# Kernel optimization log

Measured on AMD Instinct MI355X. Metric: run time of the kernel, lower is better.

Reference implementation:

```python
import jax, jax.numpy as jnp
import numpy as np

B, W, F = 32, 100, 128   # batch, window_size, n_features
KSIZE = 7                # conv kernel size
EMB = 8                  # embedding dim for feature-similarity matrix
ALPHA = 0.2              # leaky relu negative slope


def setup_inputs() -> dict:
    key = jax.random.key(0)
    ks = jax.random.split(key, 10)
    s = 0.05
    return {
        "x": jax.random.normal(ks[0], (B, W, F), jnp.float32),
        # ConvLayer: Conv1d(F, F, KSIZE) with 'same' padding
        "conv_w": jax.random.normal(ks[1], (F, F, KSIZE), jnp.float32) * s,
        "conv_b": jnp.zeros((F,), jnp.float32),
        # TemporalAttentionLayer (GATv2): lin(2F -> 2F), a (2F,1), bias (W,W)
        "temp_lin_w": jax.random.normal(ks[2], (2 * F, 2 * F), jnp.float32) * s,
        "temp_lin_b": jnp.zeros((2 * F,), jnp.float32),
        "temp_a": jax.random.normal(ks[3], (2 * F, 1), jnp.float32) * s,
        "temp_bias": jnp.zeros((W, W), jnp.float32),
        # FeatureAttentionLayer (GATv2): lin(2W -> 2W), a (2W,1), bias (F,F)
        "feat_lin_w": jax.random.normal(ks[4], (2 * W, 2 * W), jnp.float32) * s,
        "feat_lin_b": jnp.zeros((2 * W,), jnp.float32),
        "feat_a": jax.random.normal(ks[5], (2 * W, 1), jnp.float32) * s,
        "feat_bias": jnp.zeros((F, F), jnp.float32),
        # nn.Embedding(F, EMB) table (indexed by arange(F) -> just the table)
        "emb": jax.random.normal(ks[6], (F, EMB), jnp.float32),
        # forecasting model: Linear(W, 1) + tanh
        "fc_w": jax.random.normal(ks[7], (1, W), jnp.float32) * s,
        "fc_b": jnp.zeros((1,), jnp.float32),
    }


def _pos_encode(x):
    # pe = sin(pos*div) + cos(pos*div), div = exp(arange(F) * -ln(1e4)/F)
    pos = jnp.arange(W, dtype=jnp.float32)[:, None]
    div = jnp.exp(jnp.arange(F, dtype=jnp.float32) * (-np.log(10000.0) / F))
    pe = jnp.sin(pos * div) + jnp.cos(pos * div)  # (W, F)
    return x + pe[None]


def _conv(x, w, b):
    # x: (B, W, F) -> Conv1d over time with channels = features, 'same' length
    xc = x.transpose(0, 2, 1)  # (B, F, W)
    pad = (KSIZE - 1) // 2
    y = jax.lax.conv_general_dilated(
        xc, w, window_strides=(1,), padding=[(pad, pad)],
        dimension_numbers=("NCW", "OIW", "NCW"))
    y = jax.nn.relu(y + b[None, :, None])
    return y.transpose(0, 2, 1)  # (B, W, F)


def _gat_v2(v, lin_w, lin_b, a, bias):
    # v: (B, K, D). Equivalent to lin(concat(v_i, v_j)) via split weights +
    # broadcast add (avoids the O(K^2) concat materialization).
    D = v.shape[-1]
    left = v @ lin_w[:, :D].T    # (B, K, E) -- v_i part
    right = v @ lin_w[:, D:].T   # (B, K, E) -- v_j part
    s = left[:, :, None, :] + right[:, None, :, :] + lin_b  # (B, K, K, E)
    s = jnp.where(s >= 0, s, ALPHA * s)  # leaky relu
    e = jnp.einsum("bije,e->bij", s, a[:, 0]) + bias  # (B, K, K)
    att = jax.nn.softmax(e, axis=2)
    return jnp.tanh(jnp.einsum("bij,bjd->bid", att, v))


def reference(x, conv_w, conv_b, temp_lin_w, temp_lin_b, temp_a, temp_bias,
              feat_lin_w, feat_lin_b, feat_a, feat_bias, emb, fc_w, fc_b):
    x = _pos_encode(x)                 # (B, W, F)
    x = _conv(x, conv_w, conv_b)       # (B, W, F)
    # temporal attention: nodes = time steps
    x = _gat_v2(x, temp_lin_w, temp_lin_b, temp_a, temp_bias)  # (B, W, F)
    # feature attention: nodes = features
    xf = x.transpose(0, 2, 1)          # (B, F, W)
    xf = _gat_v2(xf, feat_lin_w, feat_lin_b, feat_a, feat_bias)
    x = xf.transpose(0, 2, 1)          # (B, W, F)
    # cosine-similarity mixing over features
    norms = jnp.linalg.norm(emb, axis=-1)
    cos = (emb @ emb.T) / (norms[:, None] * norms[None, :])  # (F, F)
    x = x @ cos.T                      # (B, W, F)
    xp = x.transpose(0, 2, 1)          # (B, F, W)
    pred = jnp.tanh(xp @ fc_w.T + fc_b)  # (B, F, 1)
    return pred.transpose(0, 2, 1)     # (B, 1, F)
```

## Files before the change

### kernel.cpp

```cpp
#include <hip/hip_runtime.h>
#include <math.h>

#define BB 32
#define WW 100
#define FF 128
#define KS 7
#define ET 256
#define EF 200



__global__ void k_prep(const float* __restrict__ cw, const float* __restrict__ tlw,
                       const float* __restrict__ flw, float* __restrict__ wt,
                       float* __restrict__ tlwT, float* __restrict__ flwT) {
    int id = blockIdx.x * 256 + threadIdx.x;
    if (id < KS * FF * FF) {
        int o = id & (FF - 1);
        int r = id >> 7;
        int k = r % KS;
        int i = r / KS;
        wt[id] = cw[(o * FF + i) * KS + k];
    }
    if (id < ET * ET) {
        int e = id & (ET - 1);
        int d = id >> 8;
        tlwT[id] = tlw[e * ET + d];
    }
    if (id < EF * EF) {
        int e = id % EF;
        int d = id / EF;
        flwT[id] = flw[e * EF + d];
    }
}

#define CTW 10
#define NROW 16
#define XPAD 20
__global__ __launch_bounds__(512) void k_conv(const float* __restrict__ x,
                                              const float* __restrict__ wt,
                                              const float* __restrict__ cb,
                                              float* __restrict__ x2) {
    int b = blockIdx.x & 31;
    int tile = blockIdx.x >> 5;
    int w0 = tile * CTW;
    int tid = threadIdx.x;
    int o = tid & (FF - 1);
    int h = tid >> 7;
    __shared__ float xs[FF][XPAD];
    __shared__ float part[4][CTW][FF];
    for (int idx = tid; idx < NROW * FF; idx += 512) {
        int r = idx >> 7, f = idx & (FF - 1);
        int t = w0 - 3 + r;
        float v = 0.f;
        if ((unsigned)t < WW) {
            float div = __expf((float)f * (-9.210340371976184f / (float)FF));
            float arg = (float)t * div;
            v = x[(b * WW + t) * FF + f] + __sinf(arg) + __cosf(arg);
        }
        xs[f][r] = v;
    }
    __syncthreads();
    float acc[CTW];
#pragma unroll
    for (int t = 0; t < CTW; ++t) acc[t] = 0.f;
    const float* wbase = wt + (h * 32) * KS * FF + o;
#pragma unroll 2
    for (int il = 0; il < 32; ++il) {
        int i = h * 32 + il;
        float4 X0 = *(const float4*)&xs[i][0];
        float4 X1 = *(const float4*)&xs[i][4];
        float4 X2 = *(const float4*)&xs[i][8];
        float4 X3 = *(const float4*)&xs[i][12];
        float xr[16] = {X0.x, X0.y, X0.z, X0.w, X1.x, X1.y, X1.z, X1.w,
                        X2.x, X2.y, X2.z, X2.w, X3.x, X3.y, X3.z, X3.w};
        const float* wp = wbase + il * KS * FF;
#pragma unroll
        for (int k = 0; k < KS; ++k) {
            float wv = wp[k * FF];
#pragma unroll
            for (int t = 0; t < CTW; ++t) acc[t] += xr[t + k] * wv;
        }
    }
#pragma unroll
    for (int t = 0; t < CTW; ++t) part[h][t][o] = acc[t];
    __syncthreads();
    for (int idx = tid; idx < CTW * FF; idx += 512) {
        int t = idx >> 7, oo = idx & (FF - 1);
        float s = part[0][t][oo] + part[1][t][oo] + part[2][t][oo] +
                  part[3][t][oo] + cb[oo];
        x2[(b * WW + w0 + t) * FF + oo] = fmaxf(s, 0.f);
    }
}

__global__ __launch_bounds__(512) void k_lr_t(const float* __restrict__ x2,
                                              const float* __restrict__ tlwT,
                                              const float* __restrict__ tlb,
                                              float* __restrict__ LT,
                                              float* __restrict__ Rt) {
    int b = blockIdx.x & 31;
    int tile = blockIdx.x >> 5;
    int i0 = tile * 8;
    int tid = threadIdx.x;
    int e = tid & 255;
    int rh = tid >> 8;
    __shared__ float xs[8][FF];
    for (int idx = tid; idx < 8 * FF; idx += 512) {
        int r = idx >> 7, d = idx & (FF - 1);
        int row = i0 + r; if (row >= WW) row = WW - 1;
        xs[r][d] = x2[(b * WW + row) * FF + d];
    }
    __syncthreads();
    float aL[4] = {0, 0, 0, 0}, aR[4] = {0, 0, 0, 0};
    const float* wl = tlwT + e;
#pragma unroll 2
    for (int dc = 0; dc < 32; ++dc) {
        float xv[4][4];
#pragma unroll
        for (int r = 0; r < 4; ++r)
            *(float4*)xv[r] = *(const float4*)&xs[rh * 4 + r][dc * 4];
#pragma unroll
        for (int q = 0; q < 4; ++q) {
            int d = dc * 4 + q;
            float wL = wl[d * ET];
            float wR = wl[(FF + d) * ET];
#pragma unroll
            for (int r = 0; r < 4; ++r) {
                aL[r] += xv[r][q] * wL;
                aR[r] += xv[r][q] * wR;
            }
        }
    }
    int ibase = i0 + rh * 4;
    if (ibase < WW) {
        float lb = tlb[e];
        float o0[4];
#pragma unroll
        for (int r = 0; r < 4; ++r) o0[r] = aL[r] + lb;
        *(float4*)&LT[(b * ET + e) * WW + ibase] = *(float4*)o0;
        *(float4*)&Rt[(b * ET + e) * WW + ibase] = *(float4*)aR;
    }
}

__global__ __launch_bounds__(512) void k_att_t(const float* __restrict__ LT,
                                               const float* __restrict__ Rt,
                                               const float* __restrict__ ta,
                                               const float* __restrict__ tbias,
                                               const float* __restrict__ x2,
                                               float* __restrict__ x3T) {
    int b = blockIdx.x & 31;
    int tile = blockIdx.x >> 5;
    int i0 = tile * 8;
    int tid = threadIdx.x;
    int j = tid & 127, g = tid >> 7;
    __shared__ float Rs[32][FF];
    __shared__ float Ls[32][8];
    __shared__ float tas[ET];
    __shared__ float attQ[8][FF];
    __shared__ float ob[8][FF];
    __shared__ float redA[8][2], redB[8][2];
    if (tid < ET) tas[tid] = ta[tid];
    float s0 = 0.f, s1 = 0.f;
    for (int ch = 0; ch < 8; ++ch) {
        int e0 = ch * 32;
#pragma unroll
        for (int it = 0; it < 8; ++it) {
            int idx = tid + it * 512;
            int er = idx >> 7, w = idx & 127;
            Rs[er][w] = (w < WW) ? Rt[(b * ET + e0 + er) * WW + w] : 0.f;
        }
        if (tid < 256) {
            int er = tid >> 3, qq = tid & 7;
            int row = i0 + qq; if (row >= WW) row = WW - 1;
            Ls[er][qq] = LT[(b * ET + e0 + er) * WW + row];
        }
        __syncthreads();
#pragma unroll 8
        for (int e = 0; e < 32; ++e) {
            float rj = Rs[e][j];
            float ae = tas[e0 + e];
            float2 lv = *(const float2*)&Ls[e][g * 2];
            float v;
            v = lv.x + rj; v = fmaxf(v, 0.2f * v); s0 += v * ae;
            v = lv.y + rj; v = fmaxf(v, 0.2f * v); s1 += v * ae;
        }
        __syncthreads();
    }
    float ej[2];
#pragma unroll
    for (int ii = 0; ii < 2; ++ii) {
        int i = i0 + g * 2 + ii;
        float sv = (ii == 0) ? s0 : s1;
        float bv = (j < WW && i < WW) ? tbias[i * WW + j] : 0.f;
        ej[ii] = (j < WW && i < WW) ? sv + bv : -1e30f;
    }
    float m[2] = {ej[0], ej[1]};
#pragma unroll
    for (int off = 32; off > 0; off >>= 1) {
#pragma unroll
        for (int ii = 0; ii < 2; ++ii) m[ii] = fmaxf(m[ii], __shfl_xor(m[ii], off));
    }
    int wv = tid >> 6;
    if ((tid & 63) == 0) { redA[wv][0] = m[0]; redA[wv][1] = m[1]; }
    __syncthreads();
    float p[2], ps[2];
#pragma unroll
    for (int ii = 0; ii < 2; ++ii) {
        float mx = fmaxf(redA[g * 2][ii], redA[g * 2 + 1][ii]);
        p[ii] = (j < WW) ? __expf(ej[ii] - mx) : 0.f;
        ps[ii] = p[ii];
    }
#pragma unroll
    for (int off = 32; off > 0; off >>= 1) {
#pragma unroll
        for (int ii = 0; ii < 2; ++ii) ps[ii] += __shfl_xor(ps[ii], off);
    }
    if ((tid & 63) == 0) { redB[wv][0] = ps[0]; redB[wv][1] = ps[1]; }
    __syncthreads();
#pragma unroll
    for (int ii = 0; ii < 2; ++ii) {
        float inv = 1.f / (redB[g * 2][ii] + redB[g * 2 + 1][ii]);
        attQ[g * 2 + ii][j] = p[ii] * inv;
    }
    int d = tid & 127, ph = tid >> 7;
    float pv0 = 0.f, pv1 = 0.f;
    const float* a0 = attQ[ph * 2];
    const float* a1 = attQ[ph * 2 + 1];
    for (int jc = 0; jc < 4; ++jc) {
        __syncthreads();
        for (int idx = tid; idx < 25 * FF; idx += 512) {
            int r = idx >> 7, f = idx & 127;
            Rs[r][f] = x2[(b * WW + jc * 25 + r) * FF + f];
        }
        __syncthreads();
#pragma unroll 5
        for (int r = 0; r < 25; ++r) {
            float xv = Rs[r][d];
            pv0 += a0[jc * 25 + r] * xv;
            pv1 += a1[jc * 25 + r] * xv;
        }
    }
    ob[ph * 2][d] = tanhf(pv0);
    ob[ph * 2 + 1][d] = tanhf(pv1);
    __syncthreads();
    if (tid < 256) {
        int f = tid >> 1, half = tid & 1;
        if (i0 + half * 4 < WW) {
            float4 v = make_float4(ob[half * 4][f], ob[half * 4 + 1][f],
                                   ob[half * 4 + 2][f], ob[half * 4 + 3][f]);
            *(float4*)&x3T[(b * FF + f) * WW + i0 + half * 4] = v;
        }
    }
}

__global__ __launch_bounds__(512) void k_lr_f(const float* __restrict__ x3T,
                                              const float* __restrict__ flwT,
                                              const float* __restrict__ flb,
                                              float* __restrict__ LfT,
                                              float* __restrict__ RfT) {
    int b = blockIdx.x & 31;
    int tile = blockIdx.x >> 5;
    int f0 = tile * 8;
    int tid = threadIdx.x;
    int e = tid & 255;
    int rh = tid >> 8;
    __shared__ float xs[8][WW];
    for (int idx = tid; idx < 8 * WW; idx += 512) {
        int r = idx / WW, d = idx % WW;
        xs[r][d] = x3T[(b * FF + f0 + r) * WW + d];
    }
    __syncthreads();
    if (e < EF) {
        float aL[4] = {0, 0, 0, 0}, aR[4] = {0, 0, 0, 0};
        const float* wl = flwT + e;
#pragma unroll 2
        for (int dc = 0; dc < 25; ++dc) {
            float xv[4][4];
#pragma unroll
            for (int r = 0; r < 4; ++r)
                *(float4*)xv[r] = *(const float4*)&xs[rh * 4 + r][dc * 4];
#pragma unroll
            for (int q = 0; q < 4; ++q) {
                int d = dc * 4 + q;
                float wL = wl[d * EF];
                float wR = wl[(WW + d) * EF];
#pragma unroll
                for (int r = 0; r < 4; ++r) {
                    aL[r] += xv[r][q] * wL;
                    aR[r] += xv[r][q] * wR;
                }
            }
        }
        float lb = flb[e];
        float o0[4];
#pragma unroll
        for (int r = 0; r < 4; ++r) o0[r] = aL[r] + lb;
        int fbase = f0 + rh * 4;
        *(float4*)&LfT[(b * EF + e) * FF + fbase] = *(float4*)o0;
        *(float4*)&RfT[(b * EF + e) * FF + fbase] = *(float4*)aR;
    }
}

__global__ __launch_bounds__(512) void k_att_f(const float* __restrict__ LfT,
                                               const float* __restrict__ RfT,
                                               const float* __restrict__ fa,
                                               const float* __restrict__ fbias,
                                               const float* __restrict__ x3T,
                                               const float* __restrict__ fcw,
                                               float* __restrict__ tj) {
    int b = blockIdx.x & 31;
    int tile = blockIdx.x >> 5;
    int f0 = tile * 8;
    int tid = threadIdx.x;
    int j = tid & 127, g = tid >> 7;
    __shared__ float Rs[32][FF];
    __shared__ float Ls[25][8];
    __shared__ float fas[EF];
    __shared__ float attQ[8][FF];
    __shared__ float redA[8][2], redB[8][2], redT[8][2];
    if (tid < EF) fas[tid] = fa[tid];
    float s0 = 0.f, s1 = 0.f;
    for (int ch = 0; ch < 8; ++ch) {
        int e0 = ch * 25;
        for (int idx = tid; idx < 25 * FF; idx += 512) {
            int er = idx >> 7, f = idx & 127;
            Rs[er][f] = RfT[(b * EF + e0 + er) * FF + f];
        }
        if (tid < 200) {
            int er = tid >> 3, qq = tid & 7;
            Ls[er][qq] = LfT[(b * EF + e0 + er) * FF + f0 + qq];
        }
        __syncthreads();
#pragma unroll 5
        for (int e = 0; e < 25; ++e) {
            float rj = Rs[e][j];
            float ae = fas[e0 + e];
            float2 lv = *(const float2*)&Ls[e][g * 2];
            float v;
            v = lv.x + rj; v = fmaxf(v, 0.2f * v); s0 += v * ae;
            v = lv.y + rj; v = fmaxf(v, 0.2f * v); s1 += v * ae;
        }
        __syncthreads();
    }
    float ej[2] = {s0 + fbias[(f0 + g * 2) * FF + j],
                   s1 + fbias[(f0 + g * 2 + 1) * FF + j]};
    float m[2] = {ej[0], ej[1]};
#pragma unroll
    for (int off = 32; off > 0; off >>= 1) {
#pragma unroll
        for (int ii = 0; ii < 2; ++ii) m[ii] = fmaxf(m[ii], __shfl_xor(m[ii], off));
    }
    int wv = tid >> 6;
    if ((tid & 63) == 0) { redA[wv][0] = m[0]; redA[wv][1] = m[1]; }
    __syncthreads();
    float p[2], ps[2];
#pragma unroll
    for (int ii = 0; ii < 2; ++ii) {
        float mx = fmaxf(redA[g * 2][ii], redA[g * 2 + 1][ii]);
        p[ii] = __expf(ej[ii] - mx);
        ps[ii] = p[ii];
    }
#pragma unroll
    for (int off = 32; off > 0; off >>= 1) {
#pragma unroll
        for (int ii = 0; ii < 2; ++ii) ps[ii] += __shfl_xor(ps[ii], off);
    }
    if ((tid & 63) == 0) { redB[wv][0] = ps[0]; redB[wv][1] = ps[1]; }
    __syncthreads();
#pragma unroll
    for (int ii = 0; ii < 2; ++ii) {
        float inv = 1.f / (redB[g * 2][ii] + redB[g * 2 + 1][ii]);
        attQ[g * 2 + ii][j] = p[ii] * inv;
    }
    int w = tid & 127, ph = tid >> 7;
    float pv0 = 0.f, pv1 = 0.f;
    const float* a0 = attQ[ph * 2];
    const float* a1 = attQ[ph * 2 + 1];
    for (int jc = 0; jc < 4; ++jc) {
        __syncthreads();
#pragma unroll
        for (int it = 0; it < 8; ++it) {
            int idx = tid + it * 512;
            int r = idx >> 7, ww = idx & 127;
            Rs[r][ww] = (ww < WW) ? x3T[(b * FF + jc * 32 + r) * WW + ww] : 0.f;
        }
        __syncthreads();
#pragma unroll 8
        for (int r = 0; r < 32; ++r) {
            float xv = Rs[r][w];
            pv0 += a0[jc * 32 + r] * xv;
            pv1 += a1[jc * 32 + r] * xv;
        }
    }
    bool wok = (w < WW);
    float fcv = wok ? fcw[w] : 0.f;
    float tv[2] = {tanhf(pv0) * fcv, tanhf(pv1) * fcv};
#pragma unroll
    for (int off = 32; off > 0; off >>= 1) {
#pragma unroll
        for (int ii = 0; ii < 2; ++ii) tv[ii] += __shfl_xor(tv[ii], off);
    }
    if ((tid & 63) == 0) { redT[wv][0] = tv[0]; redT[wv][1] = tv[1]; }
    __syncthreads();
    if (tid < 8) {
        int q = tid, php = q >> 1, ii = q & 1;
        tj[b * FF + f0 + q] = redT[php * 2][ii] + redT[php * 2 + 1][ii];
    }
}

__global__ __launch_bounds__(128) void k_fc(const float* __restrict__ tjg,
                                            const float* __restrict__ emb,
                                            const float* __restrict__ fcb,
                                            float* __restrict__ out) {
    int b = blockIdx.x;
    int f = threadIdx.x;
    __shared__ float en[FF][12];
    __shared__ float tjs[FF];
    {
        float4 e0 = *(const float4*)&emb[f * 8];
        float4 e1 = *(const float4*)&emb[f * 8 + 4];
        float n = e0.x*e0.x + e0.y*e0.y + e0.z*e0.z + e0.w*e0.w +
                  e1.x*e1.x + e1.y*e1.y + e1.z*e1.z + e1.w*e1.w;
        float rin = rsqrtf(n);
        float4 a = make_float4(e0.x*rin, e0.y*rin, e0.z*rin, e0.w*rin);
        float4 c = make_float4(e1.x*rin, e1.y*rin, e1.z*rin, e1.w*rin);
        *(float4*)&en[f][0] = a;
        *(float4*)&en[f][4] = c;
        tjs[f] = tjg[b * FF + f];
    }
    __syncthreads();
    float er[8];
#pragma unroll
    for (int k = 0; k < 8; ++k) er[k] = en[f][k];
    float acc = fcb[0];
    for (int jj = 0; jj < FF; ++jj) {
        float4 a = *(const float4*)&en[jj][0];
        float4 c = *(const float4*)&en[jj][4];
        float d8 = er[0]*a.x + er[1]*a.y + er[2]*a.z + er[3]*a.w +
                   er[4]*c.x + er[5]*c.y + er[6]*c.z + er[7]*c.w;
        acc += d8 * tjs[jj];
    }
    out[b * FF + f] = tanhf(acc);
}

extern "C" void kernel_launch(void* const* d_in, const int* in_sizes, int n_in,
                              void* d_out, int out_size, void* d_ws, size_t ws_size,
                              hipStream_t stream) {
    const float* x     = (const float*)d_in[0];
    const float* cw    = (const float*)d_in[1];
    const float* cb    = (const float*)d_in[2];
    const float* tlw   = (const float*)d_in[3];
    const float* tlb   = (const float*)d_in[4];
    const float* ta    = (const float*)d_in[5];
    const float* tbias = (const float*)d_in[6];
    const float* flw   = (const float*)d_in[7];
    const float* flb   = (const float*)d_in[8];
    const float* fa    = (const float*)d_in[9];
    const float* fbias = (const float*)d_in[10];
    const float* emb   = (const float*)d_in[11];
    const float* fcw   = (const float*)d_in[12];
    const float* fcb   = (const float*)d_in[13];
    float* out = (float*)d_out;
    float* ws = (float*)d_ws;

    float* x2   = ws + 409600;
    float* x3T  = ws + 819200;
    float* LT   = ws + 1228800;
    float* Rt   = ws + 2048000;
    float* tj   = ws + 2867200;
    float* wt   = ws + 3297280;
    float* tlwT = ws + 3411968;
    float* flwT = ws + 3477504;

    k_prep<<<448, 256, 0, stream>>>(cw, tlw, flw, wt, tlwT, flwT);
    k_conv<<<BB * 10, 512, 0, stream>>>(x, wt, cb, x2);
    k_lr_t<<<BB * 13, 512, 0, stream>>>(x2, tlwT, tlb, LT, Rt);
    k_att_t<<<BB * 13, 512, 0, stream>>>(LT, Rt, ta, tbias, x2, x3T);
    k_lr_f<<<BB * 16, 512, 0, stream>>>(x3T, flwT, flb, LT, Rt);
    k_att_f<<<BB * 16, 512, 0, stream>>>(LT, Rt, fa, fbias, x3T, fcw, tj);
    k_fc<<<BB, 128, 0, stream>>>(tj, emb, fcb, out);
}
```

Measured before the change: 127.6 us.

## Split attention score reduction across e-dimension with per-thread 8-row register tiles

In both attention kernels each thread now computes all 8 query rows for one column j over a quarter of the embedding dimension, instead of 2 rows over the full dimension. Partial sums are combined through a shared-memory buffer. The attention-times-values product gets the same treatment, reading a transposed attention matrix as float4 and reducing row partials across thread groups. This raises arithmetic per shared-memory load of Rs, at the cost of extra shared memory, extra barriers, and softmax work confined to 128 threads.

After: 138.9 us. +8.9%, slower.

```diff
diff --git a/kernel.cpp b/kernel.cpp
--- a/kernel.cpp
+++ b/kernel.cpp
@@ -7,7 +7,6 @@
 #define KS 7
 #define ET 256
 #define EF 200
-
 
 
 __global__ void k_prep(const float* __restrict__ cw, const float* __restrict__ tlw,
@@ -151,15 +150,16 @@
     int tile = blockIdx.x >> 5;
     int i0 = tile * 8;
     int tid = threadIdx.x;
-    int j = tid & 127, g = tid >> 7;
+    int j = tid & 127, eq = tid >> 7;
     __shared__ float Rs[32][FF];
     __shared__ float Ls[32][8];
     __shared__ float tas[ET];
-    __shared__ float attQ[8][FF];
+    __shared__ float sacc[4][8][128];
+    __shared__ float attQT[WW][8];
     __shared__ float ob[8][FF];
-    __shared__ float redA[8][2], redB[8][2];
+    __shared__ float redM[2][8], redS[2][8];
     if (tid < ET) tas[tid] = ta[tid];
-    float s0 = 0.f, s1 = 0.f;
+    float s[8] = {0, 0, 0, 0, 0, 0, 0, 0};
     for (int ch = 0; ch < 8; ++ch) {
         int e0 = ch * 32;
 #pragma unroll
@@ -174,57 +174,78 @@
             Ls[er][qq] = LT[(b * ET + e0 + er) * WW + row];
         }
         __syncthreads();
-#pragma unroll 8
-        for (int e = 0; e < 32; ++e) {
+#pragma unroll
+        for (int el = 0; el < 8; ++el) {
+            int e = eq * 8 + el;
             float rj = Rs[e][j];
             float ae = tas[e0 + e];
-            float2 lv = *(const float2*)&Ls[e][g * 2];
+            float4 l0 = *(const float4*)&Ls[e][0];
+            float4 l1 = *(const float4*)&Ls[e][4];
             float v;
-            v = lv.x + rj; v = fmaxf(v, 0.2f * v); s0 += v * ae;
-            v = lv.y + rj; v = fmaxf(v, 0.2f * v); s1 += v * ae;
-        }
-        __syncthreads();
-    }
-    float ej[2];
-#pragma unroll
-    for (int ii = 0; ii < 2; ++ii) {
-        int i = i0 + g * 2 + ii;
-        float sv = (ii == 0) ? s0 : s1;
-        float bv = (j < WW && i < WW) ? tbias[i * WW + j] : 0.f;
-        ej[ii] = (j < WW && i < WW) ? sv + bv : -1e30f;
-    }
-    float m[2] = {ej[0], ej[1]};
+            v = l0.x + rj; v = fmaxf(v, 0.2f * v); s[0] += v * ae;
+            v = l0.y + rj; v = fmaxf(v, 0.2f * v); s[1] += v * ae;
+            v = l0.z + rj; v = fmaxf(v, 0.2f * v); s[2] += v * ae;
+            v = l0.w + rj; v = fmaxf(v, 0.2f * v); s[3] += v * ae;
+            v = l1.x + rj; v = fmaxf(v, 0.2f * v); s[4] += v * ae;
+            v = l1.y + rj; v = fmaxf(v, 0.2f * v); s[5] += v * ae;
+            v = l1.z + rj; v = fmaxf(v, 0.2f * v); s[6] += v * ae;
+            v = l1.w + rj; v = fmaxf(v, 0.2f * v); s[7] += v * ae;
+        }
+        __syncthreads();
+    }
+#pragma unroll
+    for (int q = 0; q < 8; ++q) sacc[eq][q][j] = s[q];
+    __syncthreads();
+    bool act = tid < 128;
+    float ej[8];
+#pragma unroll
+    for (int q = 0; q < 8; ++q) {
+        float v = -1e30f;
+        if (act) {
+            int i = i0 + q;
+            v = sacc[0][q][j] + sacc[1][q][j] + sacc[2][q][j] + sacc[3][q][j];
+            v += (j < WW && i < WW) ? tbias[i * WW + j] : 0.f;
+            if (j >= WW) v = -1e30f;
+        }
+        ej[q] = v;
+    }
+    float m[8];
+#pragma unroll
+    for (int q = 0; q < 8; ++q) m[q] = ej[q];
 #pragma unroll
     for (int off = 32; off > 0; off >>= 1) {
 #pragma unroll
-        for (int ii = 0; ii < 2; ++ii) m[ii] = fmaxf(m[ii], __shfl_xor(m[ii], off));
-    }
-    int wv = tid >> 6;
-    if ((tid & 63) == 0) { redA[wv][0] = m[0]; redA[wv][1] = m[1]; }
-    __syncthreads();
-    float p[2], ps[2];
-#pragma unroll
-    for (int ii = 0; ii < 2; ++ii) {
-        float mx = fmaxf(redA[g * 2][ii], redA[g * 2 + 1][ii]);
-        p[ii] = (j < WW) ? __expf(ej[ii] - mx) : 0.f;
-        ps[ii] = p[ii];
+        for (int q = 0; q < 8; ++q) m[q] = fmaxf(m[q], __shfl_xor(m[q], off));
+    }
+    if (act && (tid & 63) == 0) {
+#pragma unroll
+        for (int q = 0; q < 8; ++q) redM[tid >> 6][q] = m[q];
+    }
+    __syncthreads();
+    float p[8], ps[8];
+#pragma unroll
+    for (int q = 0; q < 8; ++q) {
+        float mx = fmaxf(redM[0][q], redM[1][q]);
+        p[q] = (act && j < WW) ? __expf(ej[q] - mx) : 0.f;
+        ps[q] = p[q];
     }
 #pragma unroll
     for (int off = 32; off > 0; off >>= 1) {
 #pragma unroll
-        for (int ii = 0; ii < 2; ++ii) ps[ii] += __shfl_xor(ps[ii], off);
-    }
-    if ((tid & 63) == 0) { redB[wv][0] = ps[0]; redB[wv][1] = ps[1]; }
-    __syncthreads();
-#pragma unroll
-    for (int ii = 0; ii < 2; ++ii) {
-        float inv = 1.f / (redB[g * 2][ii] + redB[g * 2 + 1][ii]);
-        attQ[g * 2 + ii][j] = p[ii] * inv;
-    }
-    int d = tid & 127, ph = tid >> 7;
-    float pv0 = 0.f, pv1 = 0.f;
-    const float* a0 = attQ[ph * 2];
-    const float* a1 = attQ[ph * 2 + 1];
+        for (int q = 0; q < 8; ++q) ps[q] += __shfl_xor(ps[q], off);
+    }
+    if (act && (tid & 63) == 0) {
+#pragma unroll
+        for (int q = 0; q < 8; ++q) redS[tid >> 6][q] = ps[q];
+    }
+    __syncthreads();
+    if (act && j < WW) {
+#pragma unroll
+        for (int q = 0; q < 8; ++q)
+            attQT[j][q] = p[q] / (redS[0][q] + redS[1][q]);
+    }
+    int d = j, rq = eq;
+    float pv[8] = {0, 0, 0, 0, 0, 0, 0, 0};
     for (int jc = 0; jc < 4; ++jc) {
         __syncthreads();
         for (int idx = tid; idx < 25 * FF; idx += 512) {
@@ -232,15 +253,27 @@
             Rs[r][f] = x2[(b * WW + jc * 25 + r) * FF + f];
         }
         __syncthreads();
-#pragma unroll 5
-        for (int r = 0; r < 25; ++r) {
+        for (int r = rq; r < 25; r += 4) {
             float xv = Rs[r][d];
-            pv0 += a0[jc * 25 + r] * xv;
-            pv1 += a1[jc * 25 + r] * xv;
-        }
-    }
-    ob[ph * 2][d] = tanhf(pv0);
-    ob[ph * 2 + 1][d] = tanhf(pv1);
+            float4 a0 = *(const float4*)&attQT[jc * 25 + r][0];
+            float4 a1 = *(const float4*)&attQT[jc * 25 + r][4];
+            pv[0] += a0.x * xv; pv[1] += a0.y * xv;
+            pv[2] += a0.z * xv; pv[3] += a0.w * xv;
+            pv[4] += a1.x * xv; pv[5] += a1.y * xv;
+            pv[6] += a1.z * xv; pv[7] += a1.w * xv;
+        }
+    }
+    __syncthreads();
+#pragma unroll
+    for (int q = 0; q < 8; ++q) sacc[rq][q][d] = pv[q];
+    __syncthreads();
+    if (tid < 128) {
+#pragma unroll
+        for (int q = 0; q < 8; ++q) {
+            float v = sacc[0][q][d] + sacc[1][q][d] + sacc[2][q][d] + sacc[3][q][d];
+            ob[q][d] = tanhf(v);
+        }
+    }
     __syncthreads();
     if (tid < 256) {
         int f = tid >> 1, half = tid & 1;
@@ -311,70 +344,96 @@
     int tile = blockIdx.x >> 5;
     int f0 = tile * 8;
     int tid = threadIdx.x;
-    int j = tid & 127, g = tid >> 7;
-    __shared__ float Rs[32][FF];
-    __shared__ float Ls[25][8];
+    int j = tid & 127, eq = tid >> 7;
+    __shared__ float Rs[40][FF];
+    __shared__ float Ls[40][8];
     __shared__ float fas[EF];
-    __shared__ float attQ[8][FF];
-    __shared__ float redA[8][2], redB[8][2], redT[8][2];
+    __shared__ float sacc[4][8][128];
+    __shared__ float attQT[FF][8];
+    __shared__ float redM[2][8], redS[2][8], redT[2][8];
     if (tid < EF) fas[tid] = fa[tid];
-    float s0 = 0.f, s1 = 0.f;
-    for (int ch = 0; ch < 8; ++ch) {
-        int e0 = ch * 25;
-        for (int idx = tid; idx < 25 * FF; idx += 512) {
+    float s[8] = {0, 0, 0, 0, 0, 0, 0, 0};
+    for (int ch = 0; ch < 5; ++ch) {
+        int e0 = ch * 40;
+        for (int idx = tid; idx < 40 * FF; idx += 512) {
             int er = idx >> 7, f = idx & 127;
             Rs[er][f] = RfT[(b * EF + e0 + er) * FF + f];
         }
-        if (tid < 200) {
+        if (tid < 320) {
             int er = tid >> 3, qq = tid & 7;
             Ls[er][qq] = LfT[(b * EF + e0 + er) * FF + f0 + qq];
         }
         __syncthreads();
-#pragma unroll 5
-        for (int e = 0; e < 25; ++e) {
+#pragma unroll
+        for (int el = 0; el < 10; ++el) {
+            int e = eq * 10 + el;
             float rj = Rs[e][j];
             float ae = fas[e0 + e];
-            float2 lv = *(const float2*)&Ls[e][g * 2];
+            float4 l0 = *(const float4*)&Ls[e][0];
+            float4 l1 = *(const float4*)&Ls[e][4];
             float v;
-            v = lv.x + rj; v = fmaxf(v, 0.2f * v); s0 += v * ae;
-            v = lv.y + rj; v = fmaxf(v, 0.2f * v); s1 += v * ae;
-        }
-        __syncthreads();
-    }
-    float ej[2] = {s0 + fbias[(f0 + g * 2) * FF + j],
-                   s1 + fbias[(f0 + g * 2 + 1) * FF + j]};
-    float m[2] = {ej[0], ej[1]};
+            v = l0.x + rj; v = fmaxf(v, 0.2f * v); s[0] += v * ae;
+            v = l0.y + rj; v = fmaxf(v, 0.2f * v); s[1] += v * ae;
+            v = l0.z + rj; v = fmaxf(v, 0.2f * v); s[2] += v * ae;
+            v = l0.w + rj; v = fmaxf(v, 0.2f * v); s[3] += v * ae;
+            v = l1.x + rj; v = fmaxf(v, 0.2f * v); s[4] += v * ae;
+            v = l1.y + rj; v = fmaxf(v, 0.2f * v); s[5] += v * ae;
+            v = l1.z + rj; v = fmaxf(v, 0.2f * v); s[6] += v * ae;
+            v = l1.w + rj; v = fmaxf(v, 0.2f * v); s[7] += v * ae;
+        }
+        __syncthreads();
+    }
+#pragma unroll
+    for (int q = 0; q < 8; ++q) sacc[eq][q][j] = s[q];
+    __syncthreads();
+    bool act = tid < 128;
+    float ej[8];
+#pragma unroll
+    for (int q = 0; q < 8; ++q) {
+        float v = -1e30f;
+        if (act) {
+            v = sacc[0][q][j] + sacc[1][q][j] + sacc[2][q][j] + sacc[3][q][j];
+            v += fbias[(f0 + q) * FF + j];
+        }
+        ej[q] = v;
+    }
+    float m[8];
+#pragma unroll
+    for (int q = 0; q < 8; ++q) m[q] = ej[q];
 #pragma unroll
     for (int off = 32; off > 0; off >>= 1) {
 #pragma unroll
-        for (int ii = 0; ii < 2; ++ii) m[ii] = fmaxf(m[ii], __shfl_xor(m[ii], off));
-    }
-    int wv = tid >> 6;
-    if ((tid & 63) == 0) { redA[wv][0] = m[0]; redA[wv][1] = m[1]; }
-    __syncthreads();
-    float p[2], ps[2];
-#pragma unroll
-    for (int ii = 0; ii < 2; ++ii) {
-        float mx = fmaxf(redA[g * 2][ii], redA[g * 2 + 1][ii]);
-        p[ii] = __expf(ej[ii] - mx);
-        ps[ii] = p[ii];
+        for (int q = 0; q < 8; ++q) m[q] = fmaxf(m[q], __shfl_xor(m[q], off));
+    }
+    if (act && (tid & 63) == 0) {
+#pragma unroll
+        for (int q = 0; q < 8; ++q) redM[tid >> 6][q] = m[q];
+    }
+    __syncthreads();
+    float p[8], ps[8];
+#pragma unroll
+    for (int q = 0; q < 8; ++q) {
+        float mx = fmaxf(redM[0][q], redM[1][q]);
+        p[q] = act ? __expf(ej[q] - mx) : 0.f;
+        ps[q] = p[q];
     }
 #pragma unroll
     for (int off = 32; off > 0; off >>= 1) {
 #pragma unroll
-        for (int ii = 0; ii < 2; ++ii) ps[ii] += __shfl_xor(ps[ii], off);
-    }
-    if ((tid & 63) == 0) { redB[wv][0] = ps[0]; redB[wv][1] = ps[1]; }
-    __syncthreads();
-#pragma unroll
-    for (int ii = 0; ii < 2; ++ii) {
-        float inv = 1.f / (redB[g * 2][ii] + redB[g * 2 + 1][ii]);
-        attQ[g * 2 + ii][j] = p[ii] * inv;
-    }
-    int w = tid & 127, ph = tid >> 7;
-    float pv0 = 0.f, pv1 = 0.f;
-    const float* a0 = attQ[ph * 2];
-    const float* a1 = attQ[ph * 2 + 1];
+        for (int q = 0; q < 8; ++q) ps[q] += __shfl_xor(ps[q], off);
+    }
+    if (act && (tid & 63) == 0) {
+#pragma unroll
+        for (int q = 0; q < 8; ++q) redS[tid >> 6][q] = ps[q];
+    }
+    __syncthreads();
+    if (act) {
+#pragma unroll
+        for (int q = 0; q < 8; ++q)
+            attQT[j][q] = p[q] / (redS[0][q] + redS[1][q]);
+    }
+    int w = j, rq = eq;
+    float pv[8] = {0, 0, 0, 0, 0, 0, 0, 0};
     for (int jc = 0; jc < 4; ++jc) {
         __syncthreads();
 #pragma unroll
@@ -384,27 +443,42 @@
             Rs[r][ww] = (ww < WW) ? x3T[(b * FF + jc * 32 + r) * WW + ww] : 0.f;
         }
         __syncthreads();
-#pragma unroll 8
-        for (int r = 0; r < 32; ++r) {
+#pragma unroll
+        for (int rr = 0; rr < 8; ++rr) {
+            int r = rq * 8 + rr;
             float xv = Rs[r][w];
-            pv0 += a0[jc * 32 + r] * xv;
-            pv1 += a1[jc * 32 + r] * xv;
-        }
-    }
-    bool wok = (w < WW);
+            float4 a0 = *(const float4*)&attQT[jc * 32 + r][0];
+            float4 a1 = *(const float4*)&attQT[jc * 32 + r][4];
+            pv[0] += a0.x * xv; pv[1] += a0.y * xv;
+            pv[2] += a0.z * xv; pv[3] += a0.w * xv;
+            pv[4] += a1.x * xv; pv[5] += a1.y * xv;
+            pv[6] += a1.z * xv; pv[7] += a1.w * xv;
+        }
+    }
+    __syncthreads();
+#pragma unroll
+    for (int q = 0; q < 8; ++q) sacc[rq][q][w] = pv[q];
+    __syncthreads();
+    float tv[8];
+    bool wok = act && (w < WW);
     float fcv = wok ? fcw[w] : 0.f;
-    float tv[2] = {tanhf(pv0) * fcv, tanhf(pv1) * fcv};
+#pragma unroll
+    for (int q = 0; q < 8; ++q) {
+        float v = act ? (sacc[0][q][w] + sacc[1][q][w] + sacc[2][q][w] + sacc[3][q][w]) : 0.f;
+        tv[q] = act ? tanhf(v) * fcv : 0.f;
+    }
 #pragma unroll
     for (int off = 32; off > 0; off >>= 1) {
 #pragma unroll
-        for (int ii = 0; ii < 2; ++ii) tv[ii] += __shfl_xor(tv[ii], off);
-    }
-    if ((tid & 63) == 0) { redT[wv][0] = tv[0]; redT[wv][1] = tv[1]; }
-    __syncthreads();
-    if (tid < 8) {
-        int q = tid, php = q >> 1, ii = q & 1;
-        tj[b * FF + f0 + q] = redT[php * 2][ii] + redT[php * 2 + 1][ii];
-    }
+        for (int q = 0; q < 8; ++q) tv[q] += __shfl_xor(tv[q], off);
+    }
+    if (act && (tid & 63) == 0) {
+#pragma unroll
+        for (int q = 0; q < 8; ++q) redT[tid >> 6][q] = tv[q];
+    }
+    __syncthreads();
+    if (tid < 8)
+        tj[b * FF + f0 + tid] = redT[0][tid] + redT[1][tid];
 }
 
 __global__ __launch_bounds__(128) void k_fc(const float* __restrict__ tjg,
```

## Double-buffer shared-memory tiles with register prefetch in attention kernels

Applied to the files above, without the earlier changes.

The temporal and feature attention kernels now stage the next chunk of R/L rows and x rows into registers while the current chunk is computed from a second shared-memory buffer. This halves the barriers per chunk and overlaps global loads with the score and aggregation loops. The feature kernel also moves to 40-row chunks, and the temporal aggregation moves to 32-row chunks. The cost is more shared memory and registers per 512-thread block, which may lower occupancy.

After: 118.2 us, median of 3. 1.08x faster.

```diff
diff --git a/kernel.cpp b/kernel.cpp
--- a/kernel.cpp
+++ b/kernel.cpp
@@ -7,7 +7,6 @@
 #define KS 7
 #define ET 256
 #define EF 200
-
 
 
 __global__ void k_prep(const float* __restrict__ cw, const float* __restrict__ tlw,
@@ -152,46 +151,84 @@
     int i0 = tile * 8;
     int tid = threadIdx.x;
     int j = tid & 127, g = tid >> 7;
-    __shared__ float Rs[32][FF];
-    __shared__ float Ls[32][8];
+    __shared__ float Rs[2][32][FF];
+    __shared__ float Ls[2][32][8];
     __shared__ float tas[ET];
     __shared__ float attQ[8][FF];
     __shared__ float ob[8][FF];
     __shared__ float redA[8][2], redB[8][2];
     if (tid < ET) tas[tid] = ta[tid];
-    float s0 = 0.f, s1 = 0.f;
-    for (int ch = 0; ch < 8; ++ch) {
-        int e0 = ch * 32;
+
+    float rv[8];
+    float lvr = 0.f;
+    {
+        const float* Rb = Rt + (b * ET) * WW;
 #pragma unroll
         for (int it = 0; it < 8; ++it) {
             int idx = tid + it * 512;
             int er = idx >> 7, w = idx & 127;
-            Rs[er][w] = (w < WW) ? Rt[(b * ET + e0 + er) * WW + w] : 0.f;
+            rv[it] = (w < WW) ? Rb[er * WW + w] : 0.f;
         }
         if (tid < 256) {
             int er = tid >> 3, qq = tid & 7;
             int row = i0 + qq; if (row >= WW) row = WW - 1;
-            Ls[er][qq] = LT[(b * ET + e0 + er) * WW + row];
-        }
-        __syncthreads();
+            lvr = LT[(b * ET + er) * WW + row];
+        }
+    }
+#pragma unroll
+    for (int it = 0; it < 8; ++it) {
+        int idx = tid + it * 512;
+        Rs[0][idx >> 7][idx & 127] = rv[it];
+    }
+    if (tid < 256) Ls[0][tid >> 3][tid & 7] = lvr;
+    __syncthreads();
+
+    float s0 = 0.f, s1 = 0.f;
+    for (int ch = 0; ch < 8; ++ch) {
+        int buf = ch & 1;
+        if (ch < 7) {
+            int e0 = (ch + 1) * 32;
+            const float* Rb = Rt + (b * ET + e0) * WW;
+#pragma unroll
+            for (int it = 0; it < 8; ++it) {
+                int idx = tid + it * 512;
+                int er = idx >> 7, w = idx & 127;
+                rv[it] = (w < WW) ? Rb[er * WW + w] : 0.f;
+            }
+            if (tid < 256) {
+                int er = tid >> 3, qq = tid & 7;
+                int row = i0 + qq; if (row >= WW) row = WW - 1;
+                lvr = LT[(b * ET + e0 + er) * WW + row];
+            }
+        }
+        int e0 = ch * 32;
 #pragma unroll 8
         for (int e = 0; e < 32; ++e) {
-            float rj = Rs[e][j];
+            float rj = Rs[buf][e][j];
             float ae = tas[e0 + e];
-            float2 lv = *(const float2*)&Ls[e][g * 2];
+            float2 lv2 = *(const float2*)&Ls[buf][e][g * 2];
             float v;
-            v = lv.x + rj; v = fmaxf(v, 0.2f * v); s0 += v * ae;
-            v = lv.y + rj; v = fmaxf(v, 0.2f * v); s1 += v * ae;
+            v = lv2.x + rj; v = fmaxf(v, 0.2f * v); s0 += v * ae;
+            v = lv2.y + rj; v = fmaxf(v, 0.2f * v); s1 += v * ae;
+        }
+        if (ch < 7) {
+#pragma unroll
+            for (int it = 0; it < 8; ++it) {
+                int idx = tid + it * 512;
+                Rs[buf ^ 1][idx >> 7][idx & 127] = rv[it];
+            }
+            if (tid < 256) Ls[buf ^ 1][tid >> 3][tid & 7] = lvr;
         }
         __syncthreads();
     }
+
     float ej[2];
-#pragma unroll
-    for (int ii = 0; ii < 2; ++ii) {
-        int i = i0 + g * 2 + ii;
-        float sv = (ii == 0) ? s0 : s1;
-        float bv = (j < WW && i < WW) ? tbias[i * WW + j] : 0.f;
-        ej[ii] = (j < WW && i < WW) ? sv + bv : -1e30f;
+    {
+        int iq = i0 + g * 2;
+        float bv0 = (j < WW && iq < WW) ? tbias[iq * WW + j] : 0.f;
+        float bv1 = (j < WW && iq + 1 < WW) ? tbias[(iq + 1) * WW + j] : 0.f;
+        ej[0] = (j < WW && iq < WW) ? s0 + bv0 : -1e30f;
+        ej[1] = (j < WW && iq + 1 < WW) ? s1 + bv1 : -1e30f;
     }
     float m[2] = {ej[0], ej[1]};
 #pragma unroll
@@ -221,23 +258,51 @@
         float inv = 1.f / (redB[g * 2][ii] + redB[g * 2 + 1][ii]);
         attQ[g * 2 + ii][j] = p[ii] * inv;
     }
-    int d = tid & 127, ph = tid >> 7;
+
+    int d = j, ph = g;
     float pv0 = 0.f, pv1 = 0.f;
+#pragma unroll
+    for (int it = 0; it < 8; ++it) {
+        int idx = tid + it * 512;
+        int r = idx >> 7, f = idx & 127;
+        rv[it] = (r < WW) ? x2[(b * WW + r) * FF + f] : 0.f;
+    }
+    __syncthreads();
+#pragma unroll
+    for (int it = 0; it < 8; ++it) {
+        int idx = tid + it * 512;
+        Rs[0][idx >> 7][idx & 127] = rv[it];
+    }
+    __syncthreads();
     const float* a0 = attQ[ph * 2];
     const float* a1 = attQ[ph * 2 + 1];
     for (int jc = 0; jc < 4; ++jc) {
+        int buf = jc & 1;
+        if (jc < 3) {
+            int r0 = (jc + 1) * 32;
+#pragma unroll
+            for (int it = 0; it < 8; ++it) {
+                int idx = tid + it * 512;
+                int r = idx >> 7, f = idx & 127;
+                int row = r0 + r;
+                rv[it] = (row < WW) ? x2[(b * WW + row) * FF + f] : 0.f;
+            }
+        }
+#pragma unroll 8
+        for (int r = 0; r < 32; ++r) {
+            float xv = Rs[buf][r][d];
+            int row = jc * 32 + r;
+            pv0 += a0[row] * xv;
+            pv1 += a1[row] * xv;
+        }
+        if (jc < 3) {
+#pragma unroll
+            for (int it = 0; it < 8; ++it) {
+                int idx = tid + it * 512;
+                Rs[buf ^ 1][idx >> 7][idx & 127] = rv[it];
+            }
+        }
         __syncthreads();
-        for (int idx = tid; idx < 25 * FF; idx += 512) {
-            int r = idx >> 7, f = idx & 127;
-            Rs[r][f] = x2[(b * WW + jc * 25 + r) * FF + f];
-        }
-        __syncthreads();
-#pragma unroll 5
-        for (int r = 0; r < 25; ++r) {
-            float xv = Rs[r][d];
-            pv0 += a0[jc * 25 + r] * xv;
-            pv1 += a1[jc * 25 + r] * xv;
-        }
     }
     ob[ph * 2][d] = tanhf(pv0);
     ob[ph * 2 + 1][d] = tanhf(pv1);
@@ -312,35 +377,72 @@
     int f0 = tile * 8;
     int tid = threadIdx.x;
     int j = tid & 127, g = tid >> 7;
-    __shared__ float Rs[32][FF];
-    __shared__ float Ls[25][8];
+    __shared__ float Rs[2][40][FF];
+    __shared__ float Ls[2][40][8];
     __shared__ float fas[EF];
     __shared__ float attQ[8][FF];
     __shared__ float redA[8][2], redB[8][2], redT[8][2];
     if (tid < EF) fas[tid] = fa[tid];
+
+    float rv[10];
+    float lvr = 0.f;
+    {
+        const float* Rb = RfT + (b * EF) * FF;
+#pragma unroll
+        for (int it = 0; it < 10; ++it) {
+            int idx = tid + it * 512;
+            rv[it] = Rb[idx];
+        }
+        if (tid < 320) {
+            int er = tid >> 3, qq = tid & 7;
+            lvr = LfT[(b * EF + er) * FF + f0 + qq];
+        }
+    }
+#pragma unroll
+    for (int it = 0; it < 10; ++it) {
+        int idx = tid + it * 512;
+        Rs[0][idx >> 7][idx & 127] = rv[it];
+    }
+    if (tid < 320) Ls[0][tid >> 3][tid & 7] = lvr;
+    __syncthreads();
+
     float s0 = 0.f, s1 = 0.f;
-    for (int ch = 0; ch < 8; ++ch) {
-        int e0 = ch * 25;
-        for (int idx = tid; idx < 25 * FF; idx += 512) {
-            int er = idx >> 7, f = idx & 127;
-            Rs[er][f] = RfT[(b * EF + e0 + er) * FF + f];
-        }
-        if (tid < 200) {
-            int er = tid >> 3, qq = tid & 7;
-            Ls[er][qq] = LfT[(b * EF + e0 + er) * FF + f0 + qq];
+    for (int ch = 0; ch < 5; ++ch) {
+        int buf = ch & 1;
+        if (ch < 4) {
+            int e0 = (ch + 1) * 40;
+            const float* Rb = RfT + (b * EF + e0) * FF;
+#pragma unroll
+            for (int it = 0; it < 10; ++it) {
+                int idx = tid + it * 512;
+                rv[it] = Rb[idx];
+            }
+            if (tid < 320) {
+                int er = tid >> 3, qq = tid & 7;
+                lvr = LfT[(b * EF + e0 + er) * FF + f0 + qq];
+            }
+        }
+        int e0 = ch * 40;
+#pragma unroll 8
+        for (int e = 0; e < 40; ++e) {
+            float rj = Rs[buf][e][j];
+            float ae = fas[e0 + e];
+            float2 lv2 = *(const float2*)&Ls[buf][e][g * 2];
+            float v;
+            v = lv2.x + rj; v = fmaxf(v, 0.2f * v); s0 += v * ae;
+            v = lv2.y + rj; v = fmaxf(v, 0.2f * v); s1 += v * ae;
+        }
+        if (ch < 4) {
+#pragma unroll
+            for (int it = 0; it < 10; ++it) {
+                int idx = tid + it * 512;
+                Rs[buf ^ 1][idx >> 7][idx & 127] = rv[it];
+            }
+            if (tid < 320) Ls[buf ^ 1][tid >> 3][tid & 7] = lvr;
         }
         __syncthreads();
-#pragma unroll 5
-        for (int e = 0; e < 25; ++e) {
-            float rj = Rs[e][j];
-            float ae = fas[e0 + e];
-            float2 lv = *(const float2*)&Ls[e][g * 2];
-            float v;
-            v = lv.x + rj; v = fmaxf(v, 0.2f * v); s0 += v * ae;
-            v = lv.y + rj; v = fmaxf(v, 0.2f * v); s1 += v * ae;
-        }
-        __syncthreads();
-    }
+    }
+
     float ej[2] = {s0 + fbias[(f0 + g * 2) * FF + j],
                    s1 + fbias[(f0 + g * 2 + 1) * FF + j]};
     float m[2] = {ej[0], ej[1]};
@@ -371,25 +473,50 @@
         float inv = 1.f / (redB[g * 2][ii] + redB[g * 2 + 1][ii]);
         attQ[g * 2 + ii][j] = p[ii] * inv;
     }
-    int w = tid & 127, ph = tid >> 7;
+
+    int w = j, ph = g;
     float pv0 = 0.f, pv1 = 0.f;
+#pragma unroll
+    for (int it = 0; it < 8; ++it) {
+        int idx = tid + it * 512;
+        int r = idx >> 7, ww = idx & 127;
+        rv[it] = (ww < WW) ? x3T[(b * FF + r) * WW + ww] : 0.f;
+    }
+    __syncthreads();
+#pragma unroll
+    for (int it = 0; it < 8; ++it) {
+        int idx = tid + it * 512;
+        Rs[0][idx >> 7][idx & 127] = rv[it];
+    }
+    __syncthreads();
     const float* a0 = attQ[ph * 2];
     const float* a1 = attQ[ph * 2 + 1];
     for (int jc = 0; jc < 4; ++jc) {
-        __syncthreads();
-#pragma unroll
-        for (int it = 0; it < 8; ++it) {
-            int idx = tid + it * 512;
-            int r = idx >> 7, ww = idx & 127;
-            Rs[r][ww] = (ww < WW) ? x3T[(b * FF + jc * 32 + r) * WW + ww] : 0.f;
-        }
-        __syncthreads();
+        int buf = jc & 1;
+        if (jc < 3) {
+            int r0 = (jc + 1) * 32;
+#pragma unroll
+            for (int it = 0; it < 8; ++it) {
+                int idx = tid + it * 512;
+                int r = idx >> 7, ww = idx & 127;
+                rv[it] = (ww < WW) ? x3T[(b * FF + r0 + r) * WW + ww] : 0.f;
+            }
+        }
 #pragma unroll 8
         for (int r = 0; r < 32; ++r) {
-            float xv = Rs[r][w];
-            pv0 += a0[jc * 32 + r] * xv;
-            pv1 += a1[jc * 32 + r] * xv;
-        }
+            float xv = Rs[buf][r][w];
+            int row = jc * 32 + r;
+            pv0 += a0[row] * xv;
+            pv1 += a1[row] * xv;
+        }
+        if (jc < 3) {
+#pragma unroll
+            for (int it = 0; it < 8; ++it) {
+                int idx = tid + it * 512;
+                Rs[buf ^ 1][idx >> 7][idx & 127] = rv[it];
+            }
+        }
+        __syncthreads();
     }
     bool wok = (w < WW);
     float fcv = wok ? fcw[w] : 0.f;
```
